# Performance work log

Hardware: AMD Instinct MI355X
Metric: run time of the kernel (lower is better)

## Reference

```python
import jax, jax.numpy as jnp
import numpy as np

B, S = 2, 1024            # 2 packed sequences, equal length (offsets = [0, 1024, 2048])
HID, H = 2560, 32
D = HID // H              # 80
ROT = int(0.4 * D)        # 32 partial rotary dims
THETA = 10000.0
MAX_POS = 2048
CACHE_SLOTS = 4096


def setup_inputs() -> dict:
    key = jax.random.key(0)
    ks = jax.random.split(key, 8)
    T = B * S
    w = lambda k: jax.random.normal(k, (HID, HID), dtype=jnp.float32) * 0.02
    return {
        "h": jax.random.normal(ks[0], (T, HID), dtype=jnp.float32),
        "k_cache": jnp.zeros((CACHE_SLOTS, HID), dtype=jnp.float32),
        "v_cache": jnp.zeros((CACHE_SLOTS, HID), dtype=jnp.float32),
        "q_w": w(ks[1]), "q_b": jnp.zeros((HID,), jnp.float32),
        "k_w": w(ks[2]), "k_b": jnp.zeros((HID,), jnp.float32),
        "v_w": w(ks[3]), "v_b": jnp.zeros((HID,), jnp.float32),
        "dense_w": w(ks[4]), "dense_b": jnp.zeros((HID,), jnp.float32),
        "positions": jnp.tile(jnp.arange(S, dtype=jnp.int32), B),
        "offsets": jnp.array([0, S, 2 * S], dtype=jnp.int32),
        "cache_indices": jnp.arange(T, dtype=jnp.int32),
    }


def _rope_tables():
    # neox-style partial rotary tables, [MAX_POS, ROT//2]
    inv_freq = 1.0 / (THETA ** (jnp.arange(0, ROT, 2, dtype=jnp.float32) / ROT))
    freqs = jnp.arange(MAX_POS, dtype=jnp.float32)[:, None] * inv_freq[None, :]
    return jnp.cos(freqs), jnp.sin(freqs)


def _apply_rope(x, cos, sin):
    # x: [T, H, D]; cos/sin: [T, ROT//2] -> rotate first ROT dims, pass rest
    c = cos[:, None, :]
    s = sin[:, None, :]
    x1, x2, rest = x[..., : ROT // 2], x[..., ROT // 2 : ROT], x[..., ROT:]
    return jnp.concatenate([x1 * c - x2 * s, x2 * c + x1 * s, rest], axis=-1)


def reference(h, k_cache, v_cache, q_w, q_b, k_w, k_b, v_w, v_b,
              dense_w, dense_b, positions, offsets, cache_indices):
    T = h.shape[0]
    q = h @ q_w + q_b
    k = h @ k_w + k_b
    v = h @ v_w + v_b

    cos_t, sin_t = _rope_tables()
    cos = cos_t[positions]
    sin = sin_t[positions]
    q = _apply_rope(q.reshape(T, H, D), cos, sin)
    k = _apply_rope(k.reshape(T, H, D), cos, sin)
    v = v.reshape(T, H, D)

    # prompt_init path: scatter freshly-rotated K/V into the flat cache
    k_cache = k_cache.at[cache_indices].set(k.reshape(T, HID))
    v_cache = v_cache.at[cache_indices].set(v.reshape(T, HID))

    # packed_attention: causal attention within each (equal-length) sequence
    q4 = q.reshape(B, S, H, D)
    k4 = k.reshape(B, S, H, D)
    v4 = v.reshape(B, S, H, D)
    scale = D ** -0.5
    scores = jnp.einsum("bqhd,bkhd->bhqk", q4, k4) * scale
    causal = jnp.tril(jnp.ones((S, S), dtype=bool))
    scores = jnp.where(causal[None, None], scores, jnp.float32(-1e9))
    p = jax.nn.softmax(scores, axis=-1)
    o = jnp.einsum("bhqk,bkhd->bqhd", p, v4).reshape(T, HID)

    return o @ dense_w + dense_b
```

## Files before the change

kernel.cpp:

```cpp
#include <hip/hip_runtime.h>
#include <hip/hip_bf16.h>

#define Bq 2
#define Sq 1024
#define Tq 2048
#define HIDq 2560
#define Hq 32
#define Dq 80
#define NQKV 7680

typedef __bf16 bf16x8 __attribute__((ext_vector_type(8)));
typedef float f32x4 __attribute__((ext_vector_type(4)));
typedef unsigned short u16x8 __attribute__((ext_vector_type(8)));
using bf16 = __hip_bfloat16;

__device__ __forceinline__ void gload_lds16(const bf16* g, bf16* l) {
  __builtin_amdgcn_global_load_lds((const __attribute__((address_space(1))) void*)g,
                                   (__attribute__((address_space(3))) void*)l,
                                   16, 0, 0);
}

__global__ __launch_bounds__(256) void cast_h_kernel(const float* __restrict__ h,
                                                     bf16* __restrict__ hb) {
  int i = (blockIdx.x * 256 + threadIdx.x) * 4;
  float4 v = *(const float4*)(h + i);
  bf16 tmp[4];
  tmp[0] = __float2bfloat16(v.x);
  tmp[1] = __float2bfloat16(v.y);
  tmp[2] = __float2bfloat16(v.z);
  tmp[3] = __float2bfloat16(v.w);
  *(ushort4*)(hb + i) = *(ushort4*)tmp;
}

__global__ __launch_bounds__(256) void bias_concat_kernel(const float* __restrict__ qb,
                                                          const float* __restrict__ kb,
                                                          const float* __restrict__ vb,
                                                          float* __restrict__ bqkv) {
  int i = blockIdx.x * 256 + threadIdx.x;
  if (i < HIDq) bqkv[i] = qb[i];
  else if (i < 2 * HIDq) bqkv[i] = kb[i - HIDq];
  else bqkv[i] = vb[i - 2 * HIDq];
}

__global__ __launch_bounds__(256) void wtrans_kernel(const float* __restrict__ qw,
                                                     const float* __restrict__ kw,
                                                     const float* __restrict__ vw,
                                                     const float* __restrict__ dw,
                                                     bf16* __restrict__ wqkvt,
                                                     bf16* __restrict__ wdt) {
  __shared__ float tile[32][33];
  const int z = blockIdx.z;
  const float* src = (z == 0) ? qw : (z == 1) ? kw : (z == 2) ? vw : dw;
  const int n0 = blockIdx.x * 32;
  const int k0 = blockIdx.y * 32;
  const int tx = threadIdx.x, ty = threadIdx.y;
#pragma unroll
  for (int r = 0; r < 4; r++)
    tile[ty + 8 * r][tx] = src[(size_t)(k0 + ty + 8 * r) * HIDq + n0 + tx];
  __syncthreads();
  bf16* dst = (z < 3) ? (wqkvt + (size_t)z * HIDq * HIDq) : wdt;
#pragma unroll
  for (int r = 0; r < 4; r++)
    dst[(size_t)(n0 + ty + 8 * r) * HIDq + k0 + tx] = __float2bfloat16(tile[tx][ty + 8 * r]);
}

__global__ __launch_bounds__(512, 2) void gemm9s_kernel(const bf16* __restrict__ A,
                                                        const bf16* __restrict__ Bt,
                                                        const float* __restrict__ bias,
                                                        bf16* __restrict__ Cout,
                                                        int N, int K, int tM) {
  __shared__ char smem[9 * 16384];
  const int tid = threadIdx.x;
  const int lane = tid & 63;
  const int ln = lane & 15, lg = lane >> 4;
  const int wave = tid >> 6;
  const int wm = wave >> 2;
  const int wn = wave & 3;

  int bid = blockIdx.x, nwg = gridDim.x, swz = bid;
  if ((nwg & 7) == 0) { int cpx = nwg >> 3; swz = (bid & 7) * cpx + (bid >> 3); }
  const int m0 = (swz % tM) * 256;
  const int n0 = (swz / tM) * 256;
  const int NT = K >> 6;

  f32x4 acc[8][4];
  const f32x4 zz = {0.f, 0.f, 0.f, 0.f};
#pragma unroll
  for (int i = 0; i < 8; ++i)
#pragma unroll
    for (int j = 0; j < 4; ++j) acc[i][j] = zz;

  int srow[2], skel[2];
#pragma unroll
  for (int c = 0; c < 2; ++c) {
    const unsigned L = (unsigned)(c * 8192 + tid * 16);
    const unsigned P = L ^ (((L >> 9) & 1u) << 5);
    srow[c] = (int)(P >> 7);
    skel[c] = (int)((P & 127u) >> 1);
  }
  const int wbase = wave * 1024;

  auto STAGE = [&](int H, int ss) {
    const int hh = H & 3;
    const int th = H >> 2;
    const bf16* mat = (hh < 2) ? A : Bt;
    const int rowbase = (hh < 2) ? (m0 + hh * 128) : (n0 + (hh - 2) * 128);
    char* dst = smem + (ss << 14);
#pragma unroll
    for (int c = 0; c < 2; ++c)
      gload_lds16(mat + (size_t)(rowbase + srow[c]) * K + th * 64 + skel[c],
                  (bf16*)(dst + c * 8192 + wbase));
  };

  unsigned offA[2][4][2];
  int     halfA[2][4];
#pragma unroll
  for (int mh = 0; mh < 2; ++mh)
#pragma unroll
    for (int i = 0; i < 4; ++i) {
      const int row = wm * 128 + mh * 64 + i * 16 + ln;
      halfA[mh][i] = row >> 7;
      const int r = row & 127;
#pragma unroll
      for (int kh = 0; kh < 2; ++kh) {
        const unsigned P = (unsigned)(r * 128 + kh * 64 + lg * 16);
        offA[mh][i][kh] = P ^ (((P >> 9) & 1u) << 5);
      }
    }
  unsigned offB[4][2];
  int     halfB[4];
#pragma unroll
  for (int j = 0; j < 4; ++j) {
    const int row = wn * 64 + j * 16 + ln;
    halfB[j] = row >> 7;
    const int r = row & 127;
#pragma unroll
    for (int kh = 0; kh < 2; ++kh) {
      const unsigned P = (unsigned)(r * 128 + kh * 64 + lg * 16);
      offB[j][kh] = P ^ (((P >> 9) & 1u) << 5);
    }
  }

#pragma unroll
  for (int H = 0; H < 5; ++H) STAGE(H, H);

  int s0 = 0;
  for (int t = 0; t < NT; ++t) {
    if (t + 1 < NT) asm volatile("s_waitcnt vmcnt(2)" ::: "memory");
    else            asm volatile("s_waitcnt vmcnt(0)" ::: "memory");
    __builtin_amdgcn_s_barrier();

    int slt[4];
#pragma unroll
    for (int h = 0; h < 4; ++h) { int s = s0 + h; if (s >= 9) s -= 9; slt[h] = s << 14; }

#pragma unroll
    for (int kh = 0; kh < 2; ++kh) {
      bf16x8 bfr[4];
#pragma unroll
      for (int j = 0; j < 4; ++j)
        bfr[j] = *(const bf16x8*)(smem + slt[2 + halfB[j]] + offB[j][kh]);
#pragma unroll
      for (int mh = 0; mh < 2; ++mh) {
        {
          const int p = kh * 2 + mh;
          const int H = 4 * t + p + 5;
          if (H < 4 * NT) {
            int s = s0 + p + 5; if (s >= 9) s -= 9;
            STAGE(H, s);
          }
        }
        bf16x8 af[4];
#pragma unroll
        for (int i = 0; i < 4; ++i)
          af[i] = *(const bf16x8*)(smem + slt[halfA[mh][i]] + offA[mh][i][kh]);
        __builtin_amdgcn_s_setprio(1);
#pragma unroll
        for (int i = 0; i < 4; ++i)
#pragma unroll
          for (int j = 0; j < 4; ++j)
            acc[mh * 4 + i][j] =
                __builtin_amdgcn_mfma_f32_16x16x32_bf16(af[i], bfr[j], acc[mh * 4 + i][j], 0, 0, 0);
        __builtin_amdgcn_s_setprio(0);
      }
    }

    s0 += 4; if (s0 >= 9) s0 -= 9;
  }

#pragma unroll
  for (int i = 0; i < 8; ++i) {
    const int rowb = m0 + wm * 128 + i * 16 + lg * 4;
#pragma unroll
    for (int r = 0; r < 4; ++r) {
#pragma unroll
      for (int j = 0; j < 4; ++j) {
        const int col = n0 + wn * 64 + j * 16 + ln;
        Cout[(size_t)(rowb + r) * N + col] = __float2bfloat16(acc[i][j][r] + bias[col]);
      }
    }
  }
}

template <int MFRAG, int NFRAG, bool OUT_BF16>
__global__ __launch_bounds__(512, 4) void gemm256_kernel(const bf16* __restrict__ A,
                                                         const bf16* __restrict__ Bt,
                                                         const float* __restrict__ bias,
                                                         void* __restrict__ Cout,
                                                         int N, int K, int tMc) {
  constexpr int ACALLS = MFRAG / 4;
  constexpr int BCALLS = NFRAG / 2;
  constexpr int APANEL = 8192 * ACALLS;
  constexpr int BUFSZ = APANEL + 8192 * BCALLS;
  __shared__ char smem[3 * BUFSZ];
  const int tid = threadIdx.x;
  const int lane = tid & 63;
  const int ln = lane & 15, lg = lane >> 4;
  const int wave = tid >> 6;
  const int wm = wave >> 2;
  const int wn = wave & 3;

  int bid = blockIdx.x;
  int swz = bid;
  int nwg = gridDim.x;
  if ((nwg & 7) == 0) { int cpx = nwg >> 3; swz = (bid & 7) * cpx + (bid >> 3); }
  const int m0 = (swz % tMc) * (32 * MFRAG);
  const int n0 = (swz / tMc) * (64 * NFRAG);

  const int NT = K >> 5;

  f32x4 acc[MFRAG][NFRAG];
  const f32x4 zz = {0.f, 0.f, 0.f, 0.f};
#pragma unroll
  for (int i = 0; i < MFRAG; ++i)
#pragma unroll
    for (int j = 0; j < NFRAG; ++j) acc[i][j] = zz;

  const int Rl0 = tid >> 2;
  const int slot = tid & 3;
  const int wbase = (tid >> 6) * 1024;

  auto STAGE = [&](int t, int b) {
    const int k0 = t << 5;
    char* Ab = smem + b * BUFSZ;
    char* Bb = Ab + APANEL;
#pragma unroll
    for (int c = 0; c < ACALLS; ++c) {
      const int srow = c * 128 + Rl0;
      const int row = srow ^ ((srow >> 2) & 1);
      const int col8 = slot ^ (row & 3);
      gload_lds16(A + (size_t)(m0 + row) * K + k0 + col8 * 8,
                  (bf16*)(Ab + c * 8192 + wbase));
    }
#pragma unroll
    for (int c = 0; c < BCALLS; ++c) {
      const int srow = c * 128 + Rl0;
      const int row = srow ^ ((srow >> 2) & 1);
      const int col8 = slot ^ (row & 3);
      gload_lds16(Bt + (size_t)(n0 + row) * K + k0 + col8 * 8,
                  (bf16*)(Bb + c * 8192 + wbase));
    }
  };

  auto FRAG = [&](const char* base, int row) -> bf16x8 {
    const unsigned off = ((unsigned)((row ^ ((row >> 2) & 1)) << 6)) |
                         (((unsigned)lg << 4) ^ ((unsigned)(row & 3) << 4));
    return *(const bf16x8*)(base + off);
  };

  auto WAIT_COUNTED = [&]() {
    constexpr int NCALLS = ACALLS + BCALLS;
    if constexpr (NCALLS == 2)      asm volatile("s_waitcnt vmcnt(2)" ::: "memory");
    else if constexpr (NCALLS == 3) asm volatile("s_waitcnt vmcnt(3)" ::: "memory");
    else                            asm volatile("s_waitcnt vmcnt(4)" ::: "memory");
  };

  STAGE(0, 0);
  STAGE(1, 1);
  WAIT_COUNTED();
  __builtin_amdgcn_s_barrier();

  for (int t = 0; t < NT; ++t) {
    const int cb = t % 3;
    const char* Ab = smem + cb * BUFSZ;
    const char* Bb = Ab + APANEL;
    if (t + 2 < NT) STAGE(t + 2, (t + 2) % 3);

    bf16x8 bfr[NFRAG];
#pragma unroll
    for (int j = 0; j < NFRAG; ++j) bfr[j] = FRAG(Bb, wn * (16 * NFRAG) + j * 16 + ln);
#pragma unroll
    for (int ph = 0; ph < ACALLS; ++ph) {
      bf16x8 af[4];
#pragma unroll
      for (int i = 0; i < 4; ++i)
        af[i] = FRAG(Ab, wm * (16 * MFRAG) + (ph * 4 + i) * 16 + ln);
      __builtin_amdgcn_s_setprio(1);
#pragma unroll
      for (int i = 0; i < 4; ++i)
#pragma unroll
        for (int j = 0; j < NFRAG; ++j)
          acc[ph * 4 + i][j] =
              __builtin_amdgcn_mfma_f32_16x16x32_bf16(af[i], bfr[j], acc[ph * 4 + i][j], 0, 0, 0);
      __builtin_amdgcn_s_setprio(0);
    }

    if (t + 2 < NT) WAIT_COUNTED();
    else            asm volatile("s_waitcnt vmcnt(0)" ::: "memory");
    __builtin_amdgcn_s_barrier();
  }

#pragma unroll
  for (int i = 0; i < MFRAG; ++i) {
    const int rowb = m0 + wm * (16 * MFRAG) + i * 16 + lg * 4;
#pragma unroll
    for (int r = 0; r < 4; ++r) {
#pragma unroll
      for (int j = 0; j < NFRAG; ++j) {
        const int col = n0 + wn * (16 * NFRAG) + j * 16 + ln;
        const float v = acc[i][j][r] + bias[col];
        if (OUT_BF16)
          ((bf16*)Cout)[(size_t)(rowb + r) * N + col] = __float2bfloat16(v);
        else
          ((float*)Cout)[(size_t)(rowb + r) * N + col] = v;
      }
    }
  }
}

__global__ __launch_bounds__(256) void rope_kernel(bf16* __restrict__ qkv,
                                                   const int* __restrict__ positions) {
  int tid = blockIdx.x * 256 + threadIdx.x;
  int i = tid & 15;
  int h = (tid >> 4) & 31;
  int t = tid >> 9;
  float pos = (float)positions[t];
  float inv = exp2f(-0.83048202372f * (float)i);
  float ang = pos * inv;
  float s, c;
  sincosf(ang, &s, &c);
  size_t base = (size_t)t * NQKV + h * Dq + i;
  {
    float x1 = __bfloat162float(qkv[base]);
    float x2 = __bfloat162float(qkv[base + 16]);
    qkv[base] = __float2bfloat16(x1 * c - x2 * s);
    qkv[base + 16] = __float2bfloat16(x2 * c + x1 * s);
  }
  base += HIDq;
  {
    float x1 = __bfloat162float(qkv[base]);
    float x2 = __bfloat162float(qkv[base + 16]);
    qkv[base] = __float2bfloat16(x1 * c - x2 * s);
    qkv[base + 16] = __float2bfloat16(x2 * c + x1 * s);
  }
}

__global__ __launch_bounds__(256) void vtrans_kernel(const bf16* __restrict__ qkv,
                                                     bf16* __restrict__ vT) {
  __shared__ bf16 tile[32][33];
  const int b = blockIdx.z;
  const int c0 = blockIdx.x * 32;
  const int s0 = blockIdx.y * 32;
  const int tx = threadIdx.x, ty = threadIdx.y;
#pragma unroll
  for (int r = 0; r < 4; r++)
    tile[ty + 8 * r][tx] = qkv[(size_t)(b * Sq + s0 + ty + 8 * r) * NQKV + 2 * HIDq + c0 + tx];
  __syncthreads();
#pragma unroll
  for (int r = 0; r < 4; r++)
    vT[(size_t)b * HIDq * Sq + (size_t)(c0 + ty + 8 * r) * Sq + s0 + tx] = tile[tx][ty + 8 * r];
}

__global__ __launch_bounds__(256) void attn_kernel(const bf16* __restrict__ qkv,
                                                   const bf16* __restrict__ vT,
                                                   bf16* __restrict__ obuf) {
  const int x = blockIdx.x;
  const int p = x >> 6;
  const int hb = x & 63;
  const int h = hb >> 1;
  const int b = hb & 1;
  __shared__ bf16 Ks[64][104];
  __shared__ bf16 Vt[80][72];
  __shared__ bf16 Ps[4][16][72];
  const int tid = threadIdx.x;
  const int wave = tid >> 6, lane = tid & 63;
  const int ln = lane & 15, lg = lane >> 4;
  const float scale = 0.1118033988749895f;
  const u16x8 zv = {0, 0, 0, 0, 0, 0, 0, 0};

  u16x8 onesv = zv;
  if (ln == 0) {
#pragma unroll
    for (int e = 0; e < 8; ++e) onesv[e] = 0x3F80;
  }
  const bf16x8 bone = *(const bf16x8*)&onesv;

#pragma unroll
  for (int qsel = 0; qsel < 2; ++qsel) {
    const int qt = qsel ? (15 - p) : p;

    bf16x8 aq[3];
    {
      const size_t qbase = (size_t)(b * Sq + qt * 64 + wave * 16 + ln) * NQKV + h * Dq;
#pragma unroll
      for (int kc = 0; kc < 3; ++kc) {
        const int col = kc * 32 + lg * 8;
        u16x8 v = zv;
        if (col < 80) v = *(const u16x8*)(qkv + qbase + col);
        aq[kc] = *(bf16x8*)&v;
      }
    }

    f32x4 oacc[6];
    const f32x4 zz = {0.f, 0.f, 0.f, 0.f};
#pragma unroll
    for (int n = 0; n < 6; ++n) oacc[n] = zz;

    for (int j = 0; j <= qt; ++j) {
      const int kv0 = j * 64;
      __syncthreads();
      for (int idx = tid; idx < 64 * 13; idx += 256) {
        int rr = idx / 13, c8 = idx % 13;
        u16x8 val = zv;
        if (c8 < 10)
          val = *(const u16x8*)(qkv + (size_t)(b * Sq + kv0 + rr) * NQKV + HIDq + h * Dq + c8 * 8);
        *(u16x8*)&Ks[rr][c8 * 8] = val;
      }
      for (int idx = tid; idx < 80 * 8; idx += 256) {
        int rr = idx >> 3, c8 = idx & 7;
        *(u16x8*)&Vt[rr][c8 * 8] =
            *(const u16x8*)(vT + (size_t)b * HIDq * Sq + (size_t)(h * Dq + rr) * Sq + kv0 + c8 * 8);
      }
      __syncthreads();

      f32x4 sacc[4];
#pragma unroll
      for (int n = 0; n < 4; ++n) sacc[n] = zz;
#pragma unroll
      for (int kc = 0; kc < 3; ++kc) {
        bf16x8 bk[4];
#pragma unroll
        for (int n = 0; n < 4; ++n) bk[n] = *(const bf16x8*)&Ks[n * 16 + ln][kc * 32 + lg * 8];
#pragma unroll
        for (int n = 0; n < 4; ++n)
          sacc[n] = __builtin_amdgcn_mfma_f32_16x16x32_bf16(aq[kc], bk[n], sacc[n], 0, 0, 0);
      }

      const bool diag = (j == qt);
#pragma unroll
      for (int r = 0; r < 4; ++r) {
        const int qloc = wave * 16 + lg * 4 + r;
#pragma unroll
        for (int n = 0; n < 4; ++n) {
          float xk = sacc[n][r] * scale - 4.0f;
          if (diag && (n * 16 + ln) > qloc) xk = -__builtin_inff();
          Ps[wave][lg * 4 + r][n * 16 + ln] = __float2bfloat16(__expf(xk));
        }
      }
      asm volatile("s_waitcnt lgkmcnt(0)" ::: "memory");
      __builtin_amdgcn_sched_barrier(0);

#pragma unroll
      for (int kc = 0; kc < 2; ++kc) {
        bf16x8 ap = *(const bf16x8*)&Ps[wave][ln][kc * 32 + lg * 8];
        bf16x8 bv[5];
#pragma unroll
        for (int n = 0; n < 5; ++n) bv[n] = *(const bf16x8*)&Vt[n * 16 + ln][kc * 32 + lg * 8];
#pragma unroll
        for (int n = 0; n < 5; ++n)
          oacc[n] = __builtin_amdgcn_mfma_f32_16x16x32_bf16(ap, bv[n], oacc[n], 0, 0, 0);
        oacc[5] = __builtin_amdgcn_mfma_f32_16x16x32_bf16(ap, bone, oacc[5], 0, 0, 0);
      }
    }

#pragma unroll
    for (int r = 0; r < 4; ++r) {
      const float l = __shfl(oacc[5][r], lane & 48, 64);
      const float inv = 1.0f / l;
      const size_t rowbase =
          (size_t)(b * Sq + qt * 64 + wave * 16 + lg * 4 + r) * HIDq + h * Dq;
#pragma unroll
      for (int n5 = 0; n5 < 5; ++n5)
        obuf[rowbase + n5 * 16 + ln] = __float2bfloat16(oacc[n5][r] * inv);
    }
  }
}

extern "C" void kernel_launch(void* const* d_in, const int* in_sizes, int n_in,
                              void* d_out, int out_size, void* d_ws, size_t ws_size,
                              hipStream_t stream) {
  const float* h = (const float*)d_in[0];
  const float* q_w = (const float*)d_in[3];
  const float* q_b = (const float*)d_in[4];
  const float* k_w = (const float*)d_in[5];
  const float* k_b = (const float*)d_in[6];
  const float* v_w = (const float*)d_in[7];
  const float* v_b = (const float*)d_in[8];
  const float* dw = (const float*)d_in[9];
  const float* db = (const float*)d_in[10];
  const int* positions = (const int*)d_in[11];

  if (ws_size < 94402560ull) return;
  char* ws = (char*)d_ws;
  bf16* hb = (bf16*)(ws);
  bf16* wqkvt = (bf16*)(ws + 10485760);
  bf16* wdt = (bf16*)(ws + 49807360);
  bf16* qkv = (bf16*)(ws + 62914560);
  float* bqkv = (float*)(ws + 94371840);
  bf16* vT = hb;
  bf16* obuf = wqkvt;

  cast_h_kernel<<<5120, 256, 0, stream>>>(h, hb);
  bias_concat_kernel<<<30, 256, 0, stream>>>(q_b, k_b, v_b, bqkv);
  wtrans_kernel<<<dim3(80, 80, 4), dim3(32, 8), 0, stream>>>(q_w, k_w, v_w, dw, wqkvt, wdt);
  gemm9s_kernel<<<240, 512, 0, stream>>>(hb, wqkvt, bqkv, qkv, NQKV, HIDq, 8);
  rope_kernel<<<4096, 256, 0, stream>>>(qkv, positions);
  vtrans_kernel<<<dim3(80, 32, 2), dim3(32, 8), 0, stream>>>(qkv, vT);
  attn_kernel<<<512, 256, 0, stream>>>(qkv, vT, obuf);
  gemm256_kernel<4, 2, false><<<320, 512, 0, stream>>>(obuf, wdt, db, d_out, HIDq, HIDq, 16);
}
```

Baseline: 223.4 us.

## Share K/V tile loads between paired query tiles and prefetch next tile into registers

The attention kernel used to run its two paired query tiles (p and 15-p) one after the other, loading the K/V tiles twice. It now runs both tiles in a single KV loop, so each K/V tile loaded into LDS serves both query tiles while j <= qtA. The next tile's global loads are also issued into registers before the compute, overlapping memory latency with MFMA work. The cost is more registers for two accumulator sets and the prefetch buffers, which may lower occupancy. The zero padding of the K columns is now written once up front.

```diff
diff --git a/kernel.cpp b/kernel.cpp
--- a/kernel.cpp
+++ b/kernel.cpp
@@ -388,6 +388,9 @@
   const float scale = 0.1118033988749895f;
   const u16x8 zv = {0, 0, 0, 0, 0, 0, 0, 0};
 
+  const int qtA = p;
+  const int qtB = 15 - p;
+
   u16x8 onesv = zv;
   if (ln == 0) {
 #pragma unroll
@@ -395,44 +398,64 @@
   }
   const bf16x8 bone = *(const bf16x8*)&onesv;
 
-#pragma unroll
-  for (int qsel = 0; qsel < 2; ++qsel) {
-    const int qt = qsel ? (15 - p) : p;
-
-    bf16x8 aq[3];
+  if (tid < 128) *(u16x8*)&Ks[tid >> 1][80 + (tid & 1) * 8] = zv;
+
+  bf16x8 aqA[3], aqB[3];
+  {
+    const size_t qbA = (size_t)(b * Sq + qtA * 64 + wave * 16 + ln) * NQKV + h * Dq;
+    const size_t qbB = (size_t)(b * Sq + qtB * 64 + wave * 16 + ln) * NQKV + h * Dq;
+#pragma unroll
+    for (int kc = 0; kc < 3; ++kc) {
+      const int col = kc * 32 + lg * 8;
+      u16x8 va = zv, vb = zv;
+      if (col < 80) {
+        va = *(const u16x8*)(qkv + qbA + col);
+        vb = *(const u16x8*)(qkv + qbB + col);
+      }
+      aqA[kc] = *(bf16x8*)&va;
+      aqB[kc] = *(bf16x8*)&vb;
+    }
+  }
+
+  const bf16* kg[3]; bf16* kl[3];
+  const bf16* vg[3]; bf16* vl[3];
+#pragma unroll
+  for (int it = 0; it < 3; ++it) {
+    int c = tid + 256 * it; if (c >= 640) c = 0;
+    const int krr = c / 10, kc8 = c % 10;
+    kg[it] = qkv + (size_t)(b * Sq + krr) * NQKV + HIDq + h * Dq + kc8 * 8;
+    kl[it] = &Ks[krr][kc8 * 8];
+    const int vrr = c >> 3, vc8 = c & 7;
+    vg[it] = vT + (size_t)b * HIDq * Sq + (size_t)(h * Dq + vrr) * Sq + vc8 * 8;
+    vl[it] = &Vt[vrr][vc8 * 8];
+  }
+  const bool vld2 = (tid < 128);
+
+  u16x8 kreg[3], vreg[3];
+  kreg[0] = *(const u16x8*)kg[0]; vreg[0] = *(const u16x8*)vg[0];
+  kreg[1] = *(const u16x8*)kg[1]; vreg[1] = *(const u16x8*)vg[1];
+  if (vld2) { kreg[2] = *(const u16x8*)kg[2]; vreg[2] = *(const u16x8*)vg[2]; }
+
+  f32x4 oaccA[6], oaccB[6];
+  const f32x4 zz = {0.f, 0.f, 0.f, 0.f};
+#pragma unroll
+  for (int n = 0; n < 6; ++n) { oaccA[n] = zz; oaccB[n] = zz; }
+
+  for (int j = 0; j <= qtB; ++j) {
+    __syncthreads();
+    *(u16x8*)kl[0] = kreg[0]; *(u16x8*)vl[0] = vreg[0];
+    *(u16x8*)kl[1] = kreg[1]; *(u16x8*)vl[1] = vreg[1];
+    if (vld2) { *(u16x8*)kl[2] = kreg[2]; *(u16x8*)vl[2] = vreg[2]; }
+    if (j < qtB) {
+      const size_t ko = (size_t)(j + 1) * 64 * NQKV;
+      const int vo = (j + 1) * 64;
+      kreg[0] = *(const u16x8*)(kg[0] + ko); vreg[0] = *(const u16x8*)(vg[0] + vo);
+      kreg[1] = *(const u16x8*)(kg[1] + ko); vreg[1] = *(const u16x8*)(vg[1] + vo);
+      if (vld2) { kreg[2] = *(const u16x8*)(kg[2] + ko); vreg[2] = *(const u16x8*)(vg[2] + vo); }
+    }
+    __syncthreads();
+
     {
-      const size_t qbase = (size_t)(b * Sq + qt * 64 + wave * 16 + ln) * NQKV + h * Dq;
-#pragma unroll
-      for (int kc = 0; kc < 3; ++kc) {
-        const int col = kc * 32 + lg * 8;
-        u16x8 v = zv;
-        if (col < 80) v = *(const u16x8*)(qkv + qbase + col);
-        aq[kc] = *(bf16x8*)&v;
-      }
-    }
-
-    f32x4 oacc[6];
-    const f32x4 zz = {0.f, 0.f, 0.f, 0.f};
-#pragma unroll
-    for (int n = 0; n < 6; ++n) oacc[n] = zz;
-
-    for (int j = 0; j <= qt; ++j) {
-      const int kv0 = j * 64;
-      __syncthreads();
-      for (int idx = tid; idx < 64 * 13; idx += 256) {
-        int rr = idx / 13, c8 = idx % 13;
-        u16x8 val = zv;
-        if (c8 < 10)
-          val = *(const u16x8*)(qkv + (size_t)(b * Sq + kv0 + rr) * NQKV + HIDq + h * Dq + c8 * 8);
-        *(u16x8*)&Ks[rr][c8 * 8] = val;
-      }
-      for (int idx = tid; idx < 80 * 8; idx += 256) {
-        int rr = idx >> 3, c8 = idx & 7;
-        *(u16x8*)&Vt[rr][c8 * 8] =
-            *(const u16x8*)(vT + (size_t)b * HIDq * Sq + (size_t)(h * Dq + rr) * Sq + kv0 + c8 * 8);
-      }
-      __syncthreads();
-
       f32x4 sacc[4];
 #pragma unroll
       for (int n = 0; n < 4; ++n) sacc[n] = zz;
@@ -443,10 +466,9 @@
         for (int n = 0; n < 4; ++n) bk[n] = *(const bf16x8*)&Ks[n * 16 + ln][kc * 32 + lg * 8];
 #pragma unroll
         for (int n = 0; n < 4; ++n)
-          sacc[n] = __builtin_amdgcn_mfma_f32_16x16x32_bf16(aq[kc], bk[n], sacc[n], 0, 0, 0);
-      }
-
-      const bool diag = (j == qt);
+          sacc[n] = __builtin_amdgcn_mfma_f32_16x16x32_bf16(aqB[kc], bk[n], sacc[n], 0, 0, 0);
+      }
+      const bool diag = (j == qtB);
 #pragma unroll
       for (int r = 0; r < 4; ++r) {
         const int qloc = wave * 16 + lg * 4 + r;
@@ -459,7 +481,6 @@
       }
       asm volatile("s_waitcnt lgkmcnt(0)" ::: "memory");
       __builtin_amdgcn_sched_barrier(0);
-
 #pragma unroll
       for (int kc = 0; kc < 2; ++kc) {
         bf16x8 ap = *(const bf16x8*)&Ps[wave][ln][kc * 32 + lg * 8];
@@ -468,21 +489,65 @@
         for (int n = 0; n < 5; ++n) bv[n] = *(const bf16x8*)&Vt[n * 16 + ln][kc * 32 + lg * 8];
 #pragma unroll
         for (int n = 0; n < 5; ++n)
-          oacc[n] = __builtin_amdgcn_mfma_f32_16x16x32_bf16(ap, bv[n], oacc[n], 0, 0, 0);
-        oacc[5] = __builtin_amdgcn_mfma_f32_16x16x32_bf16(ap, bone, oacc[5], 0, 0, 0);
-      }
-    }
-
-#pragma unroll
-    for (int r = 0; r < 4; ++r) {
-      const float l = __shfl(oacc[5][r], lane & 48, 64);
-      const float inv = 1.0f / l;
-      const size_t rowbase =
-          (size_t)(b * Sq + qt * 64 + wave * 16 + lg * 4 + r) * HIDq + h * Dq;
-#pragma unroll
-      for (int n5 = 0; n5 < 5; ++n5)
-        obuf[rowbase + n5 * 16 + ln] = __float2bfloat16(oacc[n5][r] * inv);
-    }
+          oaccB[n] = __builtin_amdgcn_mfma_f32_16x16x32_bf16(ap, bv[n], oaccB[n], 0, 0, 0);
+        oaccB[5] = __builtin_amdgcn_mfma_f32_16x16x32_bf16(ap, bone, oaccB[5], 0, 0, 0);
+      }
+    }
+
+    if (j <= qtA) {
+      f32x4 sacc[4];
+#pragma unroll
+      for (int n = 0; n < 4; ++n) sacc[n] = zz;
+#pragma unroll
+      for (int kc = 0; kc < 3; ++kc) {
+        bf16x8 bk[4];
+#pragma unroll
+        for (int n = 0; n < 4; ++n) bk[n] = *(const bf16x8*)&Ks[n * 16 + ln][kc * 32 + lg * 8];
+#pragma unroll
+        for (int n = 0; n < 4; ++n)
+          sacc[n] = __builtin_amdgcn_mfma_f32_16x16x32_bf16(aqA[kc], bk[n], sacc[n], 0, 0, 0);
+      }
+      const bool diag = (j == qtA);
+#pragma unroll
+      for (int r = 0; r < 4; ++r) {
+        const int qloc = wave * 16 + lg * 4 + r;
+#pragma unroll
+        for (int n = 0; n < 4; ++n) {
+          float xk = sacc[n][r] * scale - 4.0f;
+          if (diag && (n * 16 + ln) > qloc) xk = -__builtin_inff();
+          Ps[wave][lg * 4 + r][n * 16 + ln] = __float2bfloat16(__expf(xk));
+        }
+      }
+      asm volatile("s_waitcnt lgkmcnt(0)" ::: "memory");
+      __builtin_amdgcn_sched_barrier(0);
+#pragma unroll
+      for (int kc = 0; kc < 2; ++kc) {
+        bf16x8 ap = *(const bf16x8*)&Ps[wave][ln][kc * 32 + lg * 8];
+        bf16x8 bv[5];
+#pragma unroll
+        for (int n = 0; n < 5; ++n) bv[n] = *(const bf16x8*)&Vt[n * 16 + ln][kc * 32 + lg * 8];
+#pragma unroll
+        for (int n = 0; n < 5; ++n)
+          oaccA[n] = __builtin_amdgcn_mfma_f32_16x16x32_bf16(ap, bv[n], oaccA[n], 0, 0, 0);
+        oaccA[5] = __builtin_amdgcn_mfma_f32_16x16x32_bf16(ap, bone, oaccA[5], 0, 0, 0);
+      }
+    }
+  }
+
+#pragma unroll
+  for (int r = 0; r < 4; ++r) {
+    const float lB = __shfl(oaccB[5][r], lane & 48, 64);
+    const float invB = 1.0f / lB;
+    const size_t rbB = (size_t)(b * Sq + qtB * 64 + wave * 16 + lg * 4 + r) * HIDq + h * Dq;
+#pragma unroll
+    for (int n5 = 0; n5 < 5; ++n5)
+      obuf[rbB + n5 * 16 + ln] = __float2bfloat16(oaccB[n5][r] * invB);
+    const float lA = __shfl(oaccA[5][r], lane & 48, 64);
+    const float invA = 1.0f / lA;
+    const size_t rbA = (size_t)(b * Sq + qtA * 64 + wave * 16 + lg * 4 + r) * HIDq + h * Dq;
+#pragma unroll
+    for (int n5 = 0; n5 < 5; ++n5)
+      obuf[rbA + n5 * 16 + ln] = __float2bfloat16(oaccA[n5][r] * invA);
   }
 }
 
```

Result: faster. 191.5 us, median of 2 (-14.2%).
